# Kernel tuning notes

Hardware: AMD Instinct MI355X
Metric: run time of the kernel (lower is better)

Reference implementation:

```python
import jax, jax.numpy as jnp
import numpy as np

N_LAYERS = 2
D_CONV = 4
D_MODEL = 768
D_INNER = 1536
D_STATE = 16
D_DELTA = 48
B = 2
L = 1024
EPS = 1e-5


def setup_inputs() -> dict:
    key = jax.random.key(0)
    ks = jax.random.split(key, 8)
    s = 0.02
    x = jax.random.normal(ks[0], (B, L, D_MODEL), jnp.float32)
    in_proj_w = jax.random.normal(ks[1], (N_LAYERS, 2 * D_INNER, D_MODEL), jnp.float32) * s
    conv_w = jax.random.normal(ks[2], (N_LAYERS, D_INNER, 1, D_CONV), jnp.float32) * s
    conv_b = jnp.zeros((N_LAYERS, D_INNER), jnp.float32)
    xproj_w = jax.random.normal(ks[3], (N_LAYERS, D_DELTA + 2 * D_STATE, D_INNER), jnp.float32) * s
    dt_w = jax.random.normal(ks[4], (N_LAYERS, D_INNER, D_DELTA), jnp.float32) * s
    dt_b = jax.random.normal(ks[5], (N_LAYERS, D_INNER), jnp.float32) * s
    A_log = jnp.tile(jnp.log(jnp.arange(1, D_STATE + 1, dtype=jnp.float32)), (N_LAYERS, D_INNER, 1))
    D = jnp.ones((N_LAYERS, D_INNER), jnp.float32)
    out_proj_w = jax.random.normal(ks[6], (N_LAYERS, D_MODEL, D_INNER), jnp.float32) * s
    norm_w = jnp.ones((N_LAYERS, D_MODEL), jnp.float32)
    return dict(x=x, in_proj_w=in_proj_w, conv_w=conv_w, conv_b=conv_b,
                xproj_w=xproj_w, dt_w=dt_w, dt_b=dt_b, A_log=A_log, D=D,
                out_proj_w=out_proj_w, norm_w=norm_w)


def rms_norm(x, w):
    return w * x * jax.lax.rsqrt(jnp.mean(x * x, axis=-1, keepdims=True) + EPS)


def causal_depthwise_conv(x, w, b):
    # x: [B, L, D_INNER], w: [D_INNER, 1, K], b: [D_INNER]
    xc = x.transpose(0, 2, 1)  # [B, D, L]
    y = jax.lax.conv_general_dilated(
        xc, w, window_strides=(1,), padding=[(D_CONV - 1, 0)],
        dimension_numbers=("NCH", "OIH", "NCH"), feature_group_count=D_INNER)
    y = y + b[None, :, None]
    return y.transpose(0, 2, 1)  # [B, L, D]


def ssm(x, A_log, D, xproj_w, dt_w, dt_b):
    # x: [B, L, D_INNER]
    A = -jnp.exp(A_log)  # [D, N]
    dbc = jnp.einsum('bld,ed->ble', x, xproj_w)
    delta, Bc, C = jnp.split(dbc, [D_DELTA, D_DELTA + D_STATE], axis=-1)
    delta = jax.nn.softplus(jnp.einsum('blr,dr->bld', delta, dt_w) + dt_b)  # [B, L, D]
    dA = jnp.exp(delta[..., None] * A)                          # [B, L, D, N]
    dBx = delta[..., None] * Bc[:, :, None, :] * x[..., None]   # [B, L, D, N]

    def step(h, inp):
        dA_t, dBx_t, C_t = inp
        h = dA_t * h + dBx_t                      # [B, D, N]
        y = jnp.einsum('bdn,bn->bd', h, C_t)      # [B, D]
        return h, y

    h0 = jnp.zeros((x.shape[0], D_INNER, D_STATE), x.dtype)
    _, ys = jax.lax.scan(step, h0, (dA.transpose(1, 0, 2, 3),
                                    dBx.transpose(1, 0, 2, 3),
                                    C.transpose(1, 0, 2)))
    y = ys.transpose(1, 0, 2)  # [B, L, D]
    return y + D * x


def mamba_block(x, in_w, cw, cb, xp_w, dtw, dtb, Alog, Dp, out_w):
    xz = jnp.einsum('blm,em->ble', x, in_w)           # [B, L, 2*D_INNER]
    xi, z = jnp.split(xz, 2, axis=-1)
    xi = jax.nn.silu(causal_depthwise_conv(xi, cw, cb))
    y = ssm(xi, Alog, Dp, xp_w, dtw, dtb)
    out = y * jax.nn.silu(z)
    return jnp.einsum('bld,md->blm', out, out_w)


def reference(x, in_proj_w, conv_w, conv_b, xproj_w, dt_w, dt_b, A_log, D, out_proj_w, norm_w):
    for i in range(N_LAYERS):
        x = x + mamba_block(rms_norm(x, norm_w[i]), in_proj_w[i], conv_w[i], conv_b[i],
                            xproj_w[i], dt_w[i], dt_b[i], A_log[i], D[i], out_proj_w[i])
    return x
```

## Files before the change

### kernel.cpp

```cpp
#include <hip/hip_runtime.h>
#include <hip/hip_bf16.h>
#include <cstdint>

#define NL 2
#define DM 768
#define DI 1536
#define DS 16
#define DD 48
#define DCONV 4
#define BB 2
#define LL 1024
#define MROWS (BB*LL)
#define DBCW (DD + 2*DS)
#define TC 32
#define NCH (LL/TC)
#define KSPL 4
#define XPN 128

typedef __bf16 bf16x8 __attribute__((ext_vector_type(8)));
typedef float f32x4 __attribute__((ext_vector_type(4)));
typedef ushort ushort8 __attribute__((ext_vector_type(8)));
using bf16 = __hip_bfloat16;

__device__ __forceinline__ float softplusf(float x) {
  return (x > 20.f) ? x : log1pf(__expf(x));
}

__device__ __forceinline__ float bfu2f(ushort u) {
  return __uint_as_float((uint32_t)u << 16);
}

__device__ __forceinline__ ushort f2bfu(float f) {
  const bf16 h = __float2bfloat16(f);
  return *reinterpret_cast<const ushort*>(&h);
}

__device__ __forceinline__ void load_lds16(const void* g, void* l) {
  __builtin_amdgcn_global_load_lds(
      (const __attribute__((address_space(1))) void*)g,
      (__attribute__((address_space(3))) void*)l, 16, 0, 0);
}

#define WI_N (NL*2*DI*DM)
#define WX_N (NL*XPN*DI)
#define WD_N (NL*DI*DD)
#define WO_N (NL*DM*DI)
__global__ __launch_bounds__(256)
void prep_weights(const float* __restrict__ wi, const float* __restrict__ wx,
                  const float* __restrict__ wd, const float* __restrict__ wo,
                  bf16* __restrict__ bi, bf16* __restrict__ bx,
                  bf16* __restrict__ bd, bf16* __restrict__ bo)
{
  int i = blockIdx.x * 256 + threadIdx.x;
  if (i < WI_N) { bi[i] = __float2bfloat16(wi[i]); return; }
  i -= WI_N;
  if (i < WX_N) {
    const int l = i / (XPN*DI), r = (i / DI) % XPN, k = i % DI;
    const float v = (r < DBCW) ? wx[((size_t)l*DBCW + r)*DI + k] : 0.f;
    bx[i] = __float2bfloat16(v); return;
  }
  i -= WX_N;
  if (i < WD_N) { bd[i] = __float2bfloat16(wd[i]); return; }
  i -= WD_N;
  if (i < WO_N) { bo[i] = __float2bfloat16(wo[i]); }
}

__global__ __launch_bounds__(256)
void rmsnorm_kernel(const float* __restrict__ x, const float* __restrict__ w,
                    bf16* __restrict__ out)
{
  const int row = blockIdx.x;
  const float* xr = x + (size_t)row * DM;
  const int t = threadIdx.x;
  float v0 = xr[t], v1 = xr[t + 256], v2 = xr[t + 512];
  float ss = v0*v0 + v1*v1 + v2*v2;
  #pragma unroll
  for (int off = 32; off > 0; off >>= 1) ss += __shfl_down(ss, off);
  __shared__ float sred[4];
  if ((t & 63) == 0) sred[t >> 6] = ss;
  __syncthreads();
  const float scale = rsqrtf((sred[0]+sred[1]+sred[2]+sred[3]) * (1.f/DM) + 1e-5f);
  out[(size_t)row*DM + t      ] = __float2bfloat16(v0 * scale * w[t]);
  out[(size_t)row*DM + t + 256] = __float2bfloat16(v1 * scale * w[t + 256]);
  out[(size_t)row*DM + t + 512] = __float2bfloat16(v2 * scale * w[t + 512]);
}

__global__ __launch_bounds__(256)
void gemm_in128(const bf16* __restrict__ A, const bf16* __restrict__ W,
                bf16* __restrict__ xb, bf16* __restrict__ zb)
{
  __shared__ __align__(16) bf16 As[128][32];
  __shared__ __align__(16) bf16 Ws[128][32];
  const int tid = threadIdx.x;
  const int wave = tid >> 6, lane = tid & 63;
  const int m0 = blockIdx.x * 128, n0 = blockIdx.y * 128;
  const int wr = (wave >> 1) * 64, wc = (wave & 1) * 64;
  const int l16 = lane & 15, quad = lane >> 4;
  const int srow = wave * 16 + (lane >> 2);
  const int scol = (lane & 3) * 8;
  bf16* a_base0 = &As[wave*16][0];
  bf16* a_base1 = &As[64 + wave*16][0];
  bf16* w_base0 = &Ws[wave*16][0];
  bf16* w_base1 = &Ws[64 + wave*16][0];

  f32x4 acc[4][4] = {};

  for (int k0 = 0; k0 < DM; k0 += 32) {
    load_lds16(A + (size_t)(m0 + srow) * DM + k0 + scol,      a_base0);
    load_lds16(A + (size_t)(m0 + 64 + srow) * DM + k0 + scol, a_base1);
    load_lds16(W + (size_t)(n0 + srow) * DM + k0 + scol,      w_base0);
    load_lds16(W + (size_t)(n0 + 64 + srow) * DM + k0 + scol, w_base1);
    __syncthreads();

    bf16x8 af[4], wf[4];
    #pragma unroll
    for (int i = 0; i < 4; ++i)
      af[i] = *reinterpret_cast<const bf16x8*>(&As[wr + i*16 + l16][quad*8]);
    #pragma unroll
    for (int j = 0; j < 4; ++j)
      wf[j] = *reinterpret_cast<const bf16x8*>(&Ws[wc + j*16 + l16][quad*8]);
    #pragma unroll
    for (int i = 0; i < 4; ++i)
      #pragma unroll
      for (int j = 0; j < 4; ++j)
        acc[i][j] = __builtin_amdgcn_mfma_f32_16x16x32_bf16(af[i], wf[j], acc[i][j], 0, 0, 0);
    __syncthreads();
  }

  const bool isz = (n0 >= DI);
  #pragma unroll
  for (int i = 0; i < 4; ++i) {
    #pragma unroll
    for (int j = 0; j < 4; ++j) {
      const int col = n0 + wc + j*16 + l16;
      #pragma unroll
      for (int r = 0; r < 4; ++r) {
        const int row = m0 + wr + i*16 + quad*4 + r;
        const float v = acc[i][j][r];
        if (!isz) xb[(size_t)row*DI + col]      = __float2bfloat16(v);
        else      zb[(size_t)row*DI + col - DI] = __float2bfloat16(v);
      }
    }
  }
}

template<int MODE>
__global__ __launch_bounds__(256)
void gemm64l(const bf16* __restrict__ A, int lda,
             const bf16* __restrict__ W, int ldw,
             float* __restrict__ C, int ldc, int N, int K,
             const float* __restrict__ res)
{
  __shared__ __align__(16) bf16 As[64][32];
  __shared__ __align__(16) bf16 Ws[64][32];
  const int tid = threadIdx.x;
  const int wave = tid >> 6, lane = tid & 63;
  const int m0 = blockIdx.x * 64, n0 = blockIdx.y * 64;
  const int wr = (wave >> 1) * 32, wc = (wave & 1) * 32;
  const int l16 = lane & 15, quad = lane >> 4;
  const int srow = wave * 16 + (lane >> 2);
  const int scol = (lane & 3) * 8;
  bf16* a_base = &As[wave*16][0];
  bf16* w_base = &Ws[wave*16][0];

  A += (size_t)blockIdx.z * K;
  W += (size_t)blockIdx.z * K;
  C += (size_t)blockIdx.z * MROWS * ldc;

  f32x4 acc[2][2] = {};

  for (int k0 = 0; k0 < K; k0 += 32) {
    load_lds16(A + (size_t)(m0 + srow) * lda + k0 + scol, a_base);
    load_lds16(W + (size_t)(n0 + srow) * ldw + k0 + scol, w_base);
    __syncthreads();
    bf16x8 af[2], wf[2];
    #pragma unroll
    for (int i = 0; i < 2; ++i)
      af[i] = *reinterpret_cast<const bf16x8*>(&As[wr + i*16 + l16][quad*8]);
    #pragma unroll
    for (int j = 0; j < 2; ++j)
      wf[j] = *reinterpret_cast<const bf16x8*>(&Ws[wc + j*16 + l16][quad*8]);
    #pragma unroll
    for (int i = 0; i < 2; ++i)
      #pragma unroll
      for (int j = 0; j < 2; ++j)
        acc[i][j] = __builtin_amdgcn_mfma_f32_16x16x32_bf16(af[i], wf[j], acc[i][j], 0, 0, 0);
    __syncthreads();
  }

  #pragma unroll
  for (int i = 0; i < 2; ++i) {
    #pragma unroll
    for (int j = 0; j < 2; ++j) {
      const int col = n0 + wc + j*16 + l16;
      if (col >= N) continue;
      #pragma unroll
      for (int r = 0; r < 4; ++r) {
        const int row = m0 + wr + i*16 + quad*4 + r;
        float v = acc[i][j][r];
        const size_t idx = (size_t)row * ldc + col;
        if (MODE == 3) v += res[idx];
        C[idx] = v;
      }
    }
  }
}

__global__ __launch_bounds__(256)
void conv_silu_kernel(const bf16* __restrict__ xb, const float* __restrict__ cw,
                      const float* __restrict__ cb, bf16* __restrict__ xob)
{
  const int idx = blockIdx.x * 256 + threadIdx.x;
  const int d8 = idx % (DI/8);
  const int row = idx / (DI/8);
  const int l = row % LL;
  const int d0 = d8 * 8;

  float4 cwv[8];
  #pragma unroll
  for (int j = 0; j < 8; ++j)
    cwv[j] = reinterpret_cast<const float4*>(cw)[d0 + j];

  float acc[8];
  {
    const float4* cbp = reinterpret_cast<const float4*>(cb + d0);
    float4 c0 = cbp[0], c1 = cbp[1];
    acc[0]=c0.x; acc[1]=c0.y; acc[2]=c0.z; acc[3]=c0.w;
    acc[4]=c1.x; acc[5]=c1.y; acc[6]=c1.z; acc[7]=c1.w;
  }
  #pragma unroll
  for (int k = 0; k < DCONV; ++k) {
    const int ll = l - (DCONV-1) + k;
    if (ll >= 0) {
      const ushort8 v = *reinterpret_cast<const ushort8*>(
          xb + (size_t)(row - (DCONV-1) + k) * DI + d0);
      #pragma unroll
      for (int j = 0; j < 8; ++j) {
        const float w = (k==0) ? cwv[j].x : (k==1) ? cwv[j].y : (k==2) ? cwv[j].z : cwv[j].w;
        acc[j] += w * bfu2f(v[j]);
      }
    }
  }
  ushort8 o;
  #pragma unroll
  for (int j = 0; j < 8; ++j) {
    const float s = acc[j] / (1.f + __expf(-acc[j]));
    o[j] = f2bfu(s);
  }
  *reinterpret_cast<ushort8*>(xob + (size_t)row*DI + d0) = o;
}

__global__ __launch_bounds__(256)
void gemm_dt(const float* __restrict__ xpart, const bf16* __restrict__ W,
             bf16* __restrict__ Cb, const float* __restrict__ bias)
{
  __shared__ __align__(16) bf16 As[64][40];
  __shared__ __align__(16) bf16 Ws[64][40];
  const int tid = threadIdx.x;
  const int m0 = blockIdx.x * 64, n0 = blockIdx.y * 64;
  const int wave = tid >> 6, lane = tid & 63;
  const int wr = (wave >> 1) * 32, wc = (wave & 1) * 32;
  const int l16 = lane & 15, quad = lane >> 4;
  const int srow = tid >> 2;
  const int scol = (tid & 3) * 8;

  f32x4 acc[2][2] = {};

  #pragma unroll
  for (int k0 = 0; k0 < DD; k0 += 32) {
    {
      const int cbase = k0 + scol;
      bf16* dst = &As[srow][scol];
      if (cbase < DD) {
        float a[8] = {0,0,0,0,0,0,0,0};
        #pragma unroll
        for (int z = 0; z < KSPL; ++z) {
          const float4* p = reinterpret_cast<const float4*>(
              xpart + (size_t)z*MROWS*DBCW + (size_t)(m0 + srow)*DBCW + cbase);
          const float4 u = p[0], v = p[1];
          a[0]+=u.x; a[1]+=u.y; a[2]+=u.z; a[3]+=u.w;
          a[4]+=v.x; a[5]+=v.y; a[6]+=v.z; a[7]+=v.w;
        }
        #pragma unroll
        for (int j = 0; j < 8; ++j) dst[j] = __float2bfloat16(a[j]);
      } else {
        *reinterpret_cast<uint4*>(dst) = make_uint4(0,0,0,0);
      }
    }
    {
      const bf16* src = W + (size_t)(n0 + srow) * DD + (k0 + scol);
      bf16* dst = &Ws[srow][scol];
      if (k0 + scol + 8 <= DD) {
        *reinterpret_cast<uint4*>(dst) = *reinterpret_cast<const uint4*>(src);
      } else {
        #pragma unroll
        for (int j = 0; j < 8; ++j)
          dst[j] = (k0 + scol + j < DD) ? src[j] : __float2bfloat16(0.f);
      }
    }
    __syncthreads();
    bf16x8 af[2], wf[2];
    #pragma unroll
    for (int i = 0; i < 2; ++i)
      af[i] = *reinterpret_cast<const bf16x8*>(&As[wr + i*16 + l16][quad*8]);
    #pragma unroll
    for (int j = 0; j < 2; ++j)
      wf[j] = *reinterpret_cast<const bf16x8*>(&Ws[wc + j*16 + l16][quad*8]);
    #pragma unroll
    for (int i = 0; i < 2; ++i)
      #pragma unroll
      for (int j = 0; j < 2; ++j)
        acc[i][j] = __builtin_amdgcn_mfma_f32_16x16x32_bf16(af[i], wf[j], acc[i][j], 0, 0, 0);
    __syncthreads();
  }

  #pragma unroll
  for (int i = 0; i < 2; ++i) {
    #pragma unroll
    for (int j = 0; j < 2; ++j) {
      const int col = n0 + wc + j*16 + l16;
      #pragma unroll
      for (int r = 0; r < 4; ++r) {
        const int row = m0 + wr + i*16 + quad*4 + r;
        Cb[(size_t)row*DI + col] = __float2bfloat16(softplusf(acc[i][j][r] + bias[col]));
      }
    }
  }
}

__global__ __launch_bounds__(256)
void scan_pass1(const bf16* __restrict__ delta, const bf16* __restrict__ xi,
                const float* __restrict__ xpart, const float* __restrict__ A_log,
                float* __restrict__ sdl_out, float* __restrict__ H)
{
  __shared__ float Bs[TC][DS];
  const int tid = threadIdx.x;
  const int wave = tid >> 6, lane = tid & 63;
  const int s = lane >> 5;
  const int dloc = wave*32 + (lane & 31);
  const int dt = blockIdx.x % (DI/128);
  const int c  = (blockIdx.x / (DI/128)) % NCH;
  const int b  =  blockIdx.x / ((DI/128)*NCH);
  const int d  = dt*128 + dloc;
  const int t0 = c*TC;

  for (int i = tid; i < TC*DS; i += 256) {
    const int t = i >> 4, n = i & 15;
    const size_t rb = ((size_t)b*LL + t0 + t)*DBCW + DD + n;
    float v = xpart[rb];
    #pragma unroll
    for (int z = 1; z < KSPL; ++z) v += xpart[rb + (size_t)z*(MROWS*DBCW)];
    Bs[t][n] = v;
  }

  const ushort* dptr = (const ushort*)(delta + ((size_t)b*LL + t0)*DI + d);
  const ushort* xptr = (const ushort*)(xi    + ((size_t)b*LL + t0)*DI + d);
  ushort dls[TC], xvs[TC];
  #pragma unroll
  for (int t = 0; t < TC; ++t) dls[t] = dptr[(size_t)t*DI];
  #pragma unroll
  for (int t = 0; t < TC; ++t) xvs[t] = xptr[(size_t)t*DI];

  float An[8];
  {
    const float4* ap = (const float4*)(A_log + (size_t)d*DS + s*8);
    float4 v0 = ap[0], v1 = ap[1];
    An[0] = -__expf(v0.x)*1.44269504f; An[1] = -__expf(v0.y)*1.44269504f;
    An[2] = -__expf(v0.z)*1.44269504f; An[3] = -__expf(v0.w)*1.44269504f;
    An[4] = -__expf(v1.x)*1.44269504f; An[5] = -__expf(v1.y)*1.44269504f;
    An[6] = -__expf(v1.z)*1.44269504f; An[7] = -__expf(v1.w)*1.44269504f;
  }
  __syncthreads();

  float h[8] = {0.f,0.f,0.f,0.f,0.f,0.f,0.f,0.f};
  float sacc = 0.f;
  #pragma unroll
  for (int t = 0; t < TC; ++t) {
    const float dl = bfu2f(dls[t]);
    const float xv = bfu2f(xvs[t]);
    const float dlxv = dl * xv;
    sacc += dl;
    const float4* brow = (const float4*)&Bs[t][s*8];
    const float4 b0 = brow[0], b1 = brow[1];
    const float bb[8] = {b0.x,b0.y,b0.z,b0.w,b1.x,b1.y,b1.z,b1.w};
    #pragma unroll
    for (int n = 0; n < 8; ++n) {
      const float dA = exp2f(dl * An[n]);
      h[n] = dA*h[n] + dlxv*bb[n];
    }
  }
  const size_t base = (((size_t)b*NCH + c)*DI + d)*DS + s*8;
  float4* Hp = (float4*)(H + base);
  Hp[0] = make_float4(h[0],h[1],h[2],h[3]);
  Hp[1] = make_float4(h[4],h[5],h[6],h[7]);
  if (s == 0) sdl_out[((size_t)b*NCH + c)*DI + d] = sacc;
}

__global__ __launch_bounds__(256)
void scan_fix(const float* __restrict__ sdl, const float* __restrict__ A_log,
              float* __restrict__ H)
{
  const int idx = blockIdx.x * 256 + threadIdx.x;
  const int n = idx & 15;
  const int d = (idx >> 4) % DI;
  const int b = idx / (DS * DI);
  const float An = -__expf(A_log[(size_t)d*DS + n]) * 1.44269504f;
  float hin = 0.f;
  #pragma unroll 8
  for (int c = 0; c < NCH; ++c) {
    const float Pv = exp2f(An * sdl[((size_t)b*NCH + c)*DI + d]);
    const size_t ic = (((size_t)b*NCH + c)*DI + d)*DS + n;
    const float Hv = H[ic];
    H[ic] = hin;
    hin = fmaf(Pv, hin, Hv);
  }
}

__global__ __launch_bounds__(256)
void scan_pass2(const bf16* __restrict__ delta, const bf16* __restrict__ xi,
                const float* __restrict__ xpart, const float* __restrict__ A_log,
                const float* __restrict__ H, const float* __restrict__ Dp,
                const bf16* __restrict__ zb, bf16* __restrict__ outb)
{
  __shared__ float Bs[TC][DS];
  __shared__ float Cs[TC][DS];
  const int tid = threadIdx.x;
  const int wave = tid >> 6, lane = tid & 63;
  const int s = lane >> 5;
  const int dloc = wave*32 + (lane & 31);
  const int dt = blockIdx.x % (DI/128);
  const int c  = (blockIdx.x / (DI/128)) % NCH;
  const int b  =  blockIdx.x / ((DI/128)*NCH);
  const int d  = dt*128 + dloc;
  const int t0 = c*TC;

  for (int i = tid; i < TC*2*DS; i += 256) {
    const int t = i >> 5, n32 = i & 31;
    const size_t rb = ((size_t)b*LL + t0 + t)*DBCW + DD + n32;
    float v = xpart[rb];
    #pragma unroll
    for (int z = 1; z < KSPL; ++z) v += xpart[rb + (size_t)z*(MROWS*DBCW)];
    if (n32 < DS) Bs[t][n32] = v;
    else          Cs[t][n32 - DS] = v;
  }

  const ushort* dptr = (const ushort*)(delta + ((size_t)b*LL + t0)*DI + d);
  const ushort* xptr = (const ushort*)(xi    + ((size_t)b*LL + t0)*DI + d);
  const ushort* zptr = (const ushort*)(zb    + ((size_t)b*LL + t0)*DI + d);
  ushort dls[TC], xvs[TC], zvs[TC];
  #pragma unroll
  for (int t = 0; t < TC; ++t) dls[t] = dptr[(size_t)t*DI];
  #pragma unroll
  for (int t = 0; t < TC; ++t) xvs[t] = xptr[(size_t)t*DI];
  #pragma unroll
  for (int t = 0; t < TC; ++t) zvs[t] = zptr[(size_t)t*DI];

  float An[8];
  {
    const float4* ap = (const float4*)(A_log + (size_t)d*DS + s*8);
    float4 v0 = ap[0], v1 = ap[1];
    An[0] = -__expf(v0.x)*1.44269504f; An[1] = -__expf(v0.y)*1.44269504f;
    An[2] = -__expf(v0.z)*1.44269504f; An[3] = -__expf(v0.w)*1.44269504f;
    An[4] = -__expf(v1.x)*1.44269504f; An[5] = -__expf(v1.y)*1.44269504f;
    An[6] = -__expf(v1.z)*1.44269504f; An[7] = -__expf(v1.w)*1.44269504f;
  }
  const float Dd = Dp[d];
  float h[8];
  {
    const float4* hp = (const float4*)(H + (((size_t)b*NCH + c)*DI + d)*DS + s*8);
    float4 h0 = hp[0], h1 = hp[1];
    h[0]=h0.x; h[1]=h0.y; h[2]=h0.z; h[3]=h0.w;
    h[4]=h1.x; h[5]=h1.y; h[6]=h1.z; h[7]=h1.w;
  }
  __syncthreads();

  bf16* optr = outb + ((size_t)b*LL + t0)*DI + d;

  #pragma unroll
  for (int t = 0; t < TC; ++t) {
    const float dl = bfu2f(dls[t]);
    const float xv = bfu2f(xvs[t]);
    const float zv = bfu2f(zvs[t]);
    const float dlxv = dl * xv;
    const float4* brow = (const float4*)&Bs[t][s*8];
    const float4* crow = (const float4*)&Cs[t][s*8];
    const float4 b0 = brow[0], b1 = brow[1];
    const float4 c0 = crow[0], c1 = crow[1];
    const float bb[8] = {b0.x,b0.y,b0.z,b0.w,b1.x,b1.y,b1.z,b1.w};
    const float cc[8] = {c0.x,c0.y,c0.z,c0.w,c1.x,c1.y,c1.z,c1.w};
    float y = 0.f;
    #pragma unroll
    for (int n = 0; n < 8; ++n) {
      const float dA = exp2f(dl * An[n]);
      h[n] = dA*h[n] + dlxv*bb[n];
      y = fmaf(h[n], cc[n], y);
    }
    y += __shfl_xor(y, 32);
    if (s == 0) {
      const float o = (y + Dd * xv) * (zv / (1.f + __expf(-zv)));
      optr[(size_t)t*DI] = __float2bfloat16(o);
    }
  }
}

extern "C" void kernel_launch(void* const* d_in, const int* in_sizes, int n_in,
                              void* d_out, int out_size, void* d_ws, size_t ws_size,
                              hipStream_t stream)
{
  const float* x_in   = (const float*)d_in[0];
  const float* w_inp  = (const float*)d_in[1];
  const float* w_conv = (const float*)d_in[2];
  const float* b_conv = (const float*)d_in[3];
  const float* w_xprj = (const float*)d_in[4];
  const float* w_dtp  = (const float*)d_in[5];
  const float* b_dt   = (const float*)d_in[6];
  const float* a_log  = (const float*)d_in[7];
  const float* d_par  = (const float*)d_in[8];
  const float* w_outp = (const float*)d_in[9];
  const float* w_norm = (const float*)d_in[10];
  float* xfinal = (float*)d_out;

  char* ws = (char*)d_ws;
  size_t off = 0;
  auto alloc = [&](size_t bytes) -> void* {
    void* p = ws + off;
    off += (bytes + 255) & ~(size_t)255;
    return p;
  };
  bf16*  wb_in  = (bf16*) alloc((size_t)WI_N*2);
  bf16*  wb_xp  = (bf16*) alloc((size_t)WX_N*2);
  bf16*  wb_dt  = (bf16*) alloc((size_t)WD_N*2);
  bf16*  wb_out = (bf16*) alloc((size_t)WO_N*2);
  bf16*  xn     = (bf16*) alloc((size_t)MROWS*DM*2);
  bf16*  xb     = (bf16*) alloc((size_t)MROWS*DI*2);
  bf16*  zb     = (bf16*) alloc((size_t)MROWS*DI*2);
  bf16*  xcb    = (bf16*) alloc((size_t)MROWS*DI*2);
  float* xpart  = (float*)alloc((size_t)KSPL*MROWS*DBCW*4);
  bf16*  dltb   = (bf16*) alloc((size_t)MROWS*DI*2);
  bf16*  scb    = (bf16*) alloc((size_t)MROWS*DI*2);
  float* x1     = (float*)alloc((size_t)MROWS*DM*4);
  float* sdlw   = (float*)alloc((size_t)BB*NCH*DI*4);
  float* Hws    = (float*)alloc((size_t)BB*NCH*DI*DS*4);

  prep_weights<<<(WI_N+WX_N+WD_N+WO_N + 255)/256, 256, 0, stream>>>(
      w_inp, w_xprj, w_dtp, w_outp, wb_in, wb_xp, wb_dt, wb_out);

  const float* xprev = x_in;
  for (int l = 0; l < NL; ++l) {
    rmsnorm_kernel<<<MROWS, 256, 0, stream>>>(xprev, w_norm + l*DM, xn);

    gemm_in128<<<dim3(MROWS/128, (2*DI)/128), 256, 0, stream>>>(
        xn, wb_in + (size_t)l*2*DI*DM, xb, zb);

    conv_silu_kernel<<<(MROWS*DI/8)/256, 256, 0, stream>>>(
        xb, w_conv + l*DI*DCONV, b_conv + l*DI, xcb);

    gemm64l<0><<<dim3(MROWS/64, XPN/64, KSPL), 256, 0, stream>>>(
        xcb, DI, wb_xp + (size_t)l*XPN*DI, DI, xpart, DBCW, DBCW, DI/KSPL, nullptr);

    gemm_dt<<<dim3(MROWS/64, DI/64), 256, 0, stream>>>(
        xpart, wb_dt + (size_t)l*DI*DD, dltb, b_dt + l*DI);

    scan_pass1<<<BB*NCH*(DI/128), 256, 0, stream>>>(
        dltb, xcb, xpart, a_log + (size_t)l*DI*DS, sdlw, Hws);
    scan_fix<<<(BB*DI*DS)/256, 256, 0, stream>>>(
        sdlw, a_log + (size_t)l*DI*DS, Hws);
    scan_pass2<<<BB*NCH*(DI/128), 256, 0, stream>>>(
        dltb, xcb, xpart, a_log + (size_t)l*DI*DS, Hws, d_par + l*DI, zb, scb);

    float* xout = (l == NL-1) ? xfinal : x1;
    gemm64l<3><<<dim3(MROWS/64, DM/64, 1), 256, 0, stream>>>(
        scb, DI, wb_out + (size_t)l*DM*DI, DI, xout, DM, DM, DI, xprev);

    xprev = x1;
  }
}
```

Baseline: 364.5 us.

## Fuse three scan kernels into one cooperative kernel and deepen GEMM K-step

Merges scan_pass1, scan_fix and scan_pass2 into a single cooperative kernel that uses grid-wide syncs between the chunk-local scan, the cross-chunk carry fix and the output pass. This removes two launches and keeps the delta and x chunk values in registers across phases instead of reloading them. The GEMM kernels also now stage two 32-wide K slices per barrier pair, halving the number of syncthreads. The costs are cooperative-launch occupancy limits (768 blocks must all be co-resident) and higher LDS use per block.

```diff
diff --git a/kernel.cpp b/kernel.cpp
--- a/kernel.cpp
+++ b/kernel.cpp
@@ -1,6 +1,9 @@
 #include <hip/hip_runtime.h>
 #include <hip/hip_bf16.h>
+#include <hip/hip_cooperative_groups.h>
 #include <cstdint>
+
+namespace cg = cooperative_groups;
 
 #define NL 2
 #define DM 768
@@ -89,8 +92,8 @@
 void gemm_in128(const bf16* __restrict__ A, const bf16* __restrict__ W,
                 bf16* __restrict__ xb, bf16* __restrict__ zb)
 {
-  __shared__ __align__(16) bf16 As[128][32];
-  __shared__ __align__(16) bf16 Ws[128][32];
+  __shared__ __align__(16) bf16 As[2][128][32];
+  __shared__ __align__(16) bf16 Ws[2][128][32];
   const int tid = threadIdx.x;
   const int wave = tid >> 6, lane = tid & 63;
   const int m0 = blockIdx.x * 128, n0 = blockIdx.y * 128;
@@ -98,32 +101,34 @@
   const int l16 = lane & 15, quad = lane >> 4;
   const int srow = wave * 16 + (lane >> 2);
   const int scol = (lane & 3) * 8;
-  bf16* a_base0 = &As[wave*16][0];
-  bf16* a_base1 = &As[64 + wave*16][0];
-  bf16* w_base0 = &Ws[wave*16][0];
-  bf16* w_base1 = &Ws[64 + wave*16][0];
 
   f32x4 acc[4][4] = {};
 
-  for (int k0 = 0; k0 < DM; k0 += 32) {
-    load_lds16(A + (size_t)(m0 + srow) * DM + k0 + scol,      a_base0);
-    load_lds16(A + (size_t)(m0 + 64 + srow) * DM + k0 + scol, a_base1);
-    load_lds16(W + (size_t)(n0 + srow) * DM + k0 + scol,      w_base0);
-    load_lds16(W + (size_t)(n0 + 64 + srow) * DM + k0 + scol, w_base1);
+  for (int k0 = 0; k0 < DM; k0 += 64) {
+    #pragma unroll
+    for (int kk = 0; kk < 2; ++kk) {
+      load_lds16(A + (size_t)(m0 + srow) * DM + k0 + kk*32 + scol,      &As[kk][wave*16][0]);
+      load_lds16(A + (size_t)(m0 + 64 + srow) * DM + k0 + kk*32 + scol, &As[kk][64 + wave*16][0]);
+      load_lds16(W + (size_t)(n0 + srow) * DM + k0 + kk*32 + scol,      &Ws[kk][wave*16][0]);
+      load_lds16(W + (size_t)(n0 + 64 + srow) * DM + k0 + kk*32 + scol, &Ws[kk][64 + wave*16][0]);
+    }
     __syncthreads();
 
-    bf16x8 af[4], wf[4];
-    #pragma unroll
-    for (int i = 0; i < 4; ++i)
-      af[i] = *reinterpret_cast<const bf16x8*>(&As[wr + i*16 + l16][quad*8]);
-    #pragma unroll
-    for (int j = 0; j < 4; ++j)
-      wf[j] = *reinterpret_cast<const bf16x8*>(&Ws[wc + j*16 + l16][quad*8]);
-    #pragma unroll
-    for (int i = 0; i < 4; ++i)
+    #pragma unroll
+    for (int kk = 0; kk < 2; ++kk) {
+      bf16x8 af[4], wf[4];
+      #pragma unroll
+      for (int i = 0; i < 4; ++i)
+        af[i] = *reinterpret_cast<const bf16x8*>(&As[kk][wr + i*16 + l16][quad*8]);
       #pragma unroll
       for (int j = 0; j < 4; ++j)
-        acc[i][j] = __builtin_amdgcn_mfma_f32_16x16x32_bf16(af[i], wf[j], acc[i][j], 0, 0, 0);
+        wf[j] = *reinterpret_cast<const bf16x8*>(&Ws[kk][wc + j*16 + l16][quad*8]);
+      #pragma unroll
+      for (int i = 0; i < 4; ++i)
+        #pragma unroll
+        for (int j = 0; j < 4; ++j)
+          acc[i][j] = __builtin_amdgcn_mfma_f32_16x16x32_bf16(af[i], wf[j], acc[i][j], 0, 0, 0);
+    }
     __syncthreads();
   }
 
@@ -151,8 +156,8 @@
              float* __restrict__ C, int ldc, int N, int K,
              const float* __restrict__ res)
 {
-  __shared__ __align__(16) bf16 As[64][32];
-  __shared__ __align__(16) bf16 Ws[64][32];
+  __shared__ __align__(16) bf16 As[2][64][32];
+  __shared__ __align__(16) bf16 Ws[2][64][32];
   const int tid = threadIdx.x;
   const int wave = tid >> 6, lane = tid & 63;
   const int m0 = blockIdx.x * 64, n0 = blockIdx.y * 64;
@@ -160,8 +165,6 @@
   const int l16 = lane & 15, quad = lane >> 4;
   const int srow = wave * 16 + (lane >> 2);
   const int scol = (lane & 3) * 8;
-  bf16* a_base = &As[wave*16][0];
-  bf16* w_base = &Ws[wave*16][0];
 
   A += (size_t)blockIdx.z * K;
   W += (size_t)blockIdx.z * K;
@@ -169,22 +172,28 @@
 
   f32x4 acc[2][2] = {};
 
-  for (int k0 = 0; k0 < K; k0 += 32) {
-    load_lds16(A + (size_t)(m0 + srow) * lda + k0 + scol, a_base);
-    load_lds16(W + (size_t)(n0 + srow) * ldw + k0 + scol, w_base);
+  for (int k0 = 0; k0 < K; k0 += 64) {
+    #pragma unroll
+    for (int kk = 0; kk < 2; ++kk) {
+      load_lds16(A + (size_t)(m0 + srow) * lda + k0 + kk*32 + scol, &As[kk][wave*16][0]);
+      load_lds16(W + (size_t)(n0 + srow) * ldw + k0 + kk*32 + scol, &Ws[kk][wave*16][0]);
+    }
     __syncthreads();
-    bf16x8 af[2], wf[2];
-    #pragma unroll
-    for (int i = 0; i < 2; ++i)
-      af[i] = *reinterpret_cast<const bf16x8*>(&As[wr + i*16 + l16][quad*8]);
-    #pragma unroll
-    for (int j = 0; j < 2; ++j)
-      wf[j] = *reinterpret_cast<const bf16x8*>(&Ws[wc + j*16 + l16][quad*8]);
-    #pragma unroll
-    for (int i = 0; i < 2; ++i)
+    #pragma unroll
+    for (int kk = 0; kk < 2; ++kk) {
+      bf16x8 af[2], wf[2];
+      #pragma unroll
+      for (int i = 0; i < 2; ++i)
+        af[i] = *reinterpret_cast<const bf16x8*>(&As[kk][wr + i*16 + l16][quad*8]);
       #pragma unroll
       for (int j = 0; j < 2; ++j)
-        acc[i][j] = __builtin_amdgcn_mfma_f32_16x16x32_bf16(af[i], wf[j], acc[i][j], 0, 0, 0);
+        wf[j] = *reinterpret_cast<const bf16x8*>(&Ws[kk][wc + j*16 + l16][quad*8]);
+      #pragma unroll
+      for (int i = 0; i < 2; ++i)
+        #pragma unroll
+        for (int j = 0; j < 2; ++j)
+          acc[i][j] = __builtin_amdgcn_mfma_f32_16x16x32_bf16(af[i], wf[j], acc[i][j], 0, 0, 0);
+    }
     __syncthreads();
   }
 
@@ -328,100 +337,14 @@
   }
 }
 
-__global__ __launch_bounds__(256)
-void scan_pass1(const bf16* __restrict__ delta, const bf16* __restrict__ xi,
-                const float* __restrict__ xpart, const float* __restrict__ A_log,
-                float* __restrict__ sdl_out, float* __restrict__ H)
-{
-  __shared__ float Bs[TC][DS];
-  const int tid = threadIdx.x;
-  const int wave = tid >> 6, lane = tid & 63;
-  const int s = lane >> 5;
-  const int dloc = wave*32 + (lane & 31);
-  const int dt = blockIdx.x % (DI/128);
-  const int c  = (blockIdx.x / (DI/128)) % NCH;
-  const int b  =  blockIdx.x / ((DI/128)*NCH);
-  const int d  = dt*128 + dloc;
-  const int t0 = c*TC;
-
-  for (int i = tid; i < TC*DS; i += 256) {
-    const int t = i >> 4, n = i & 15;
-    const size_t rb = ((size_t)b*LL + t0 + t)*DBCW + DD + n;
-    float v = xpart[rb];
-    #pragma unroll
-    for (int z = 1; z < KSPL; ++z) v += xpart[rb + (size_t)z*(MROWS*DBCW)];
-    Bs[t][n] = v;
-  }
-
-  const ushort* dptr = (const ushort*)(delta + ((size_t)b*LL + t0)*DI + d);
-  const ushort* xptr = (const ushort*)(xi    + ((size_t)b*LL + t0)*DI + d);
-  ushort dls[TC], xvs[TC];
-  #pragma unroll
-  for (int t = 0; t < TC; ++t) dls[t] = dptr[(size_t)t*DI];
-  #pragma unroll
-  for (int t = 0; t < TC; ++t) xvs[t] = xptr[(size_t)t*DI];
-
-  float An[8];
-  {
-    const float4* ap = (const float4*)(A_log + (size_t)d*DS + s*8);
-    float4 v0 = ap[0], v1 = ap[1];
-    An[0] = -__expf(v0.x)*1.44269504f; An[1] = -__expf(v0.y)*1.44269504f;
-    An[2] = -__expf(v0.z)*1.44269504f; An[3] = -__expf(v0.w)*1.44269504f;
-    An[4] = -__expf(v1.x)*1.44269504f; An[5] = -__expf(v1.y)*1.44269504f;
-    An[6] = -__expf(v1.z)*1.44269504f; An[7] = -__expf(v1.w)*1.44269504f;
-  }
-  __syncthreads();
-
-  float h[8] = {0.f,0.f,0.f,0.f,0.f,0.f,0.f,0.f};
-  float sacc = 0.f;
-  #pragma unroll
-  for (int t = 0; t < TC; ++t) {
-    const float dl = bfu2f(dls[t]);
-    const float xv = bfu2f(xvs[t]);
-    const float dlxv = dl * xv;
-    sacc += dl;
-    const float4* brow = (const float4*)&Bs[t][s*8];
-    const float4 b0 = brow[0], b1 = brow[1];
-    const float bb[8] = {b0.x,b0.y,b0.z,b0.w,b1.x,b1.y,b1.z,b1.w};
-    #pragma unroll
-    for (int n = 0; n < 8; ++n) {
-      const float dA = exp2f(dl * An[n]);
-      h[n] = dA*h[n] + dlxv*bb[n];
-    }
-  }
-  const size_t base = (((size_t)b*NCH + c)*DI + d)*DS + s*8;
-  float4* Hp = (float4*)(H + base);
-  Hp[0] = make_float4(h[0],h[1],h[2],h[3]);
-  Hp[1] = make_float4(h[4],h[5],h[6],h[7]);
-  if (s == 0) sdl_out[((size_t)b*NCH + c)*DI + d] = sacc;
-}
-
-__global__ __launch_bounds__(256)
-void scan_fix(const float* __restrict__ sdl, const float* __restrict__ A_log,
-              float* __restrict__ H)
-{
-  const int idx = blockIdx.x * 256 + threadIdx.x;
-  const int n = idx & 15;
-  const int d = (idx >> 4) % DI;
-  const int b = idx / (DS * DI);
-  const float An = -__expf(A_log[(size_t)d*DS + n]) * 1.44269504f;
-  float hin = 0.f;
-  #pragma unroll 8
-  for (int c = 0; c < NCH; ++c) {
-    const float Pv = exp2f(An * sdl[((size_t)b*NCH + c)*DI + d]);
-    const size_t ic = (((size_t)b*NCH + c)*DI + d)*DS + n;
-    const float Hv = H[ic];
-    H[ic] = hin;
-    hin = fmaf(Pv, hin, Hv);
-  }
-}
-
-__global__ __launch_bounds__(256)
-void scan_pass2(const bf16* __restrict__ delta, const bf16* __restrict__ xi,
-                const float* __restrict__ xpart, const float* __restrict__ A_log,
-                const float* __restrict__ H, const float* __restrict__ Dp,
-                const bf16* __restrict__ zb, bf16* __restrict__ outb)
-{
+__global__ __launch_bounds__(256, 3)
+void scan_coop(const bf16* __restrict__ delta, const bf16* __restrict__ xi,
+               const float* __restrict__ xpart, const float* __restrict__ A_log,
+               const float* __restrict__ Dp, const bf16* __restrict__ zb,
+               float* __restrict__ sdl, float* __restrict__ H,
+               bf16* __restrict__ outb)
+{
+  cg::grid_group grid = cg::this_grid();
   __shared__ float Bs[TC][DS];
   __shared__ float Cs[TC][DS];
   const int tid = threadIdx.x;
@@ -446,14 +369,11 @@
 
   const ushort* dptr = (const ushort*)(delta + ((size_t)b*LL + t0)*DI + d);
   const ushort* xptr = (const ushort*)(xi    + ((size_t)b*LL + t0)*DI + d);
-  const ushort* zptr = (const ushort*)(zb    + ((size_t)b*LL + t0)*DI + d);
-  ushort dls[TC], xvs[TC], zvs[TC];
+  ushort dls[TC], xvs[TC];
   #pragma unroll
   for (int t = 0; t < TC; ++t) dls[t] = dptr[(size_t)t*DI];
   #pragma unroll
   for (int t = 0; t < TC; ++t) xvs[t] = xptr[(size_t)t*DI];
-  #pragma unroll
-  for (int t = 0; t < TC; ++t) zvs[t] = zptr[(size_t)t*DI];
 
   float An[8];
   {
@@ -464,7 +384,58 @@
     An[4] = -__expf(v1.x)*1.44269504f; An[5] = -__expf(v1.y)*1.44269504f;
     An[6] = -__expf(v1.z)*1.44269504f; An[7] = -__expf(v1.w)*1.44269504f;
   }
-  const float Dd = Dp[d];
+  __syncthreads();
+
+  {
+    float h[8] = {0.f,0.f,0.f,0.f,0.f,0.f,0.f,0.f};
+    float sacc = 0.f;
+    #pragma unroll
+    for (int t = 0; t < TC; ++t) {
+      const float dl = bfu2f(dls[t]);
+      const float xv = bfu2f(xvs[t]);
+      const float dlxv = dl * xv;
+      sacc += dl;
+      const float4* brow = (const float4*)&Bs[t][s*8];
+      const float4 b0 = brow[0], b1 = brow[1];
+      const float bb[8] = {b0.x,b0.y,b0.z,b0.w,b1.x,b1.y,b1.z,b1.w};
+      #pragma unroll
+      for (int n = 0; n < 8; ++n) {
+        const float dA = exp2f(dl * An[n]);
+        h[n] = dA*h[n] + dlxv*bb[n];
+      }
+    }
+    const size_t base = (((size_t)b*NCH + c)*DI + d)*DS + s*8;
+    float4* Hp = (float4*)(H + base);
+    Hp[0] = make_float4(h[0],h[1],h[2],h[3]);
+    Hp[1] = make_float4(h[4],h[5],h[6],h[7]);
+    if (s == 0) sdl[((size_t)b*NCH + c)*DI + d] = sacc;
+  }
+
+  __threadfence();
+  grid.sync();
+
+  {
+    const int gid = blockIdx.x * 256 + tid;
+    if (gid < BB*DI*DS) {
+      const int n  = gid & 15;
+      const int dd = (gid >> 4) % DI;
+      const int b2 = gid / (DS * DI);
+      const float An1 = -__expf(A_log[(size_t)dd*DS + n]) * 1.44269504f;
+      float hin = 0.f;
+      #pragma unroll 8
+      for (int c2 = 0; c2 < NCH; ++c2) {
+        const float Pv = exp2f(An1 * sdl[((size_t)b2*NCH + c2)*DI + dd]);
+        const size_t ic = (((size_t)b2*NCH + c2)*DI + dd)*DS + n;
+        const float Hv = H[ic];
+        H[ic] = hin;
+        hin = fmaf(Pv, hin, Hv);
+      }
+    }
+  }
+
+  __threadfence();
+  grid.sync();
+
   float h[8];
   {
     const float4* hp = (const float4*)(H + (((size_t)b*NCH + c)*DI + d)*DS + s*8);
@@ -472,7 +443,11 @@
     h[0]=h0.x; h[1]=h0.y; h[2]=h0.z; h[3]=h0.w;
     h[4]=h1.x; h[5]=h1.y; h[6]=h1.z; h[7]=h1.w;
   }
-  __syncthreads();
+  const float Dd = Dp[d];
+  const ushort* zptr = (const ushort*)(zb + ((size_t)b*LL + t0)*DI + d);
+  ushort zvs[TC];
+  #pragma unroll
+  for (int t = 0; t < TC; ++t) zvs[t] = zptr[(size_t)t*DI];
 
   bf16* optr = outb + ((size_t)b*LL + t0)*DI + d;
 
@@ -533,7 +508,7 @@
   bf16*  wb_out = (bf16*) alloc((size_t)WO_N*2);
   bf16*  xn     = (bf16*) alloc((size_t)MROWS*DM*2);
   bf16*  xb     = (bf16*) alloc((size_t)MROWS*DI*2);
-  bf16*  zb     = (bf16*) alloc((size_t)MROWS*DI*2);
+  bf16*  zbuf   = (bf16*) alloc((size_t)MROWS*DI*2);
   bf16*  xcb    = (bf16*) alloc((size_t)MROWS*DI*2);
   float* xpart  = (float*)alloc((size_t)KSPL*MROWS*DBCW*4);
   bf16*  dltb   = (bf16*) alloc((size_t)MROWS*DI*2);
@@ -550,7 +525,7 @@
     rmsnorm_kernel<<<MROWS, 256, 0, stream>>>(xprev, w_norm + l*DM, xn);
 
     gemm_in128<<<dim3(MROWS/128, (2*DI)/128), 256, 0, stream>>>(
-        xn, wb_in + (size_t)l*2*DI*DM, xb, zb);
+        xn, wb_in + (size_t)l*2*DI*DM, xb, zbuf);
 
     conv_silu_kernel<<<(MROWS*DI/8)/256, 256, 0, stream>>>(
         xb, w_conv + l*DI*DCONV, b_conv + l*DI, xcb);
@@ -561,12 +536,22 @@
     gemm_dt<<<dim3(MROWS/64, DI/64), 256, 0, stream>>>(
         xpart, wb_dt + (size_t)l*DI*DD, dltb, b_dt + l*DI);
 
-    scan_pass1<<<BB*NCH*(DI/128), 256, 0, stream>>>(
-        dltb, xcb, xpart, a_log + (size_t)l*DI*DS, sdlw, Hws);
-    scan_fix<<<(BB*DI*DS)/256, 256, 0, stream>>>(
-        sdlw, a_log + (size_t)l*DI*DS, Hws);
-    scan_pass2<<<BB*NCH*(DI/128), 256, 0, stream>>>(
-        dltb, xcb, xpart, a_log + (size_t)l*DI*DS, Hws, d_par + l*DI, zb, scb);
+    {
+      const bf16* a0 = dltb;
+      const bf16* a1 = xcb;
+      const float* a2 = xpart;
+      const float* a3 = a_log + (size_t)l*DI*DS;
+      const float* a4 = d_par + (size_t)l*DI;
+      const bf16* a5 = zbuf;
+      float* a6 = sdlw;
+      float* a7 = Hws;
+      bf16* a8 = scb;
+      void* cargs[] = {(void*)&a0,(void*)&a1,(void*)&a2,(void*)&a3,(void*)&a4,
+                       (void*)&a5,(void*)&a6,(void*)&a7,(void*)&a8};
+      hipLaunchCooperativeKernel((void*)scan_coop,
+                                 dim3(BB*NCH*(DI/128)), dim3(256),
+                                 cargs, 0, stream);
+    }
 
     float* xout = (l == NL-1) ? xfinal : x1;
     gemm64l<3><<<dim3(MROWS/64, DM/64, 1), 256, 0, stream>>>(
```

New measurement: 1.205 ms. 231% more time.
